# Kernel optimization log

Hardware: AMD Instinct MI355X
Metric: run time of the kernel (lower is better)

Reference implementation:

```python
import jax, jax.numpy as jnp
import numpy as np
from jax import lax

NSTEPS = 7
BN_EPS = 1e-5


def setup_inputs() -> dict:
    key = jax.random.key(0)
    ks = jax.random.split(key, 7)
    bs, in_ch, h, w, k = 8, 16, 256, 256, 3
    f = jax.random.normal(ks[0], (bs, in_ch, h, w), dtype=jnp.float32)
    vec_w = jax.random.normal(ks[1], (2 * in_ch, in_ch, k, k), dtype=jnp.float32) * 0.1
    vec_b = jax.random.normal(ks[2], (2 * in_ch,), dtype=jnp.float32) * 0.1
    bn_gamma = jnp.ones((2 * in_ch,), dtype=jnp.float32)
    bn_beta = jnp.zeros((2 * in_ch,), dtype=jnp.float32)
    fuse_w = jax.random.normal(ks[3], (in_ch, in_ch, NSTEPS, 1, 1), dtype=jnp.float32) * 0.1
    fuse_b = jax.random.normal(ks[4], (in_ch,), dtype=jnp.float32) * 0.1
    return {"f": f, "vec_w": vec_w, "vec_b": vec_b, "bn_gamma": bn_gamma,
            "bn_beta": bn_beta, "fuse_w": fuse_w, "fuse_b": fuse_b}


def _bilinear_sample(src, py, px):
    """Bilinear sample with zero padding (torch grid_sample align_corners=True).
    src: [N,C,H,W]; py,px: [N,H,W] pixel coordinates (row, col)."""
    N, C, H, W = src.shape
    y0 = jnp.floor(py); x0 = jnp.floor(px)
    wy1 = py - y0; wy0 = 1.0 - wy1
    wx1 = px - x0; wx0 = 1.0 - wx1
    src_flat = src.reshape(N, C, H * W)

    def gather(yi, xi):
        valid = (yi >= 0) & (yi <= H - 1) & (xi >= 0) & (xi <= W - 1)
        yc = jnp.clip(yi, 0, H - 1).astype(jnp.int32)
        xc = jnp.clip(xi, 0, W - 1).astype(jnp.int32)
        idx = (yc * W + xc).reshape(N, 1, H * W)
        vals = jnp.take_along_axis(src_flat, idx, axis=2).reshape(N, C, H, W)
        return vals * valid.astype(src.dtype)[:, None, :, :]

    out = (wy0 * wx0)[:, None] * gather(y0, x0) \
        + (wy0 * wx1)[:, None] * gather(y0, x0 + 1) \
        + (wy1 * wx0)[:, None] * gather(y0 + 1, x0) \
        + (wy1 * wx1)[:, None] * gather(y0 + 1, x0 + 1)
    return out


def _warp(src, flow, grid_y, grid_x):
    # grid + flow in pixel space; original normalizes to [-1,1] then grid_sample
    # un-normalizes with align_corners=True, which is exactly pixel coords grid+flow.
    py = grid_y[None] + flow[:, 0]
    px = grid_x[None] + flow[:, 1]
    return _bilinear_sample(src, py, px)


def reference(f, vec_w, vec_b, bn_gamma, bn_beta, fuse_w, fuse_b):
    bs, in_ch, h, w = f.shape
    # vec_conv + BatchNorm2d (training-mode batch stats, biased variance)
    vec = lax.conv_general_dilated(f, vec_w, (1, 1), [(1, 1), (1, 1)],
                                   dimension_numbers=("NCHW", "OIHW", "NCHW"))
    vec = vec + vec_b[None, :, None, None]
    mean = vec.mean(axis=(0, 2, 3))
    var = vec.var(axis=(0, 2, 3))
    vec = bn_gamma[None, :, None, None] * (vec - mean[None, :, None, None]) \
        * lax.rsqrt(var + BN_EPS)[None, :, None, None] + bn_beta[None, :, None, None]

    c = vec.shape[1]  # = 2*in_ch
    vec = vec.reshape(bs * c // 2, 2, h, w)  # per-channel 2D flow fields

    grid_y, grid_x = jnp.meshgrid(jnp.arange(h, dtype=f.dtype),
                                  jnp.arange(w, dtype=f.dtype), indexing="ij")

    # VecInt: scaling and squaring, keeping every intermediate deformation
    vec = vec * (1.0 / 2 ** NSTEPS)
    deforms = []
    for _ in range(NSTEPS):
        vec = vec + _warp(vec, vec, grid_y, grid_x)
        deforms.append(vec)

    fsrc = f.reshape(bs * in_ch, 1, h, w)
    maps = [_warp(fsrc, d, grid_y, grid_x).reshape(bs, in_ch, h, w) for d in deforms]
    stacked = jnp.stack(maps, axis=2)  # [bs, in_ch, nsteps, h, w]

    # Conv3d with kernel (nsteps,1,1) then squeeze -> per-pixel channel/step mix
    out = jnp.einsum("ocs,bcshw->bohw", fuse_w[:, :, :, 0, 0], stacked)
    out = out + fuse_b[None, :, None, None]
    return out
```

## Files before the change

kernel.cpp:

```cpp
#include <hip/hip_runtime.h>
#include <hip/hip_fp16.h>

#define H 256
#define W 256
#define BS 8
#define IC 16
#define OCH 32
#define NSTEPS 7
#define PLANE (H*W)
#define NFIELDS (BS*IC)
#define BN_N (BS*PLANE)
#define BN_EPS 1e-5f

__global__ void transpose_w_kernel(const float* __restrict__ w,
                                   float* __restrict__ wT) {
    for (int idx = threadIdx.x; idx < OCH * IC * 9; idx += blockDim.x) {
        int oc  = idx / (IC * 9);
        int rem = idx - oc * (IC * 9);
        wT[rem * OCH + oc] = w[idx];
    }
}

__global__ __launch_bounds__(256, 4) void conv_kernel(
    const float* __restrict__ f, const float* __restrict__ wT,
    const float* __restrict__ vec_b, __half2* __restrict__ vec_out,
    __half* __restrict__ f16c) {
    __shared__ float sf[8][18][34];

    int blk = blockIdx.x;
    int xcd = blk & 7;
    int i   = blk >> 3;
    int b   = i >> 4;
    int j   = i & 15;
    int ty0 = ((xcd << 1) | (j >> 3)) * 16;
    int tx0 = (j & 7) * 32;
    int tid = threadIdx.x;
    int tyl = tid >> 5, txl = tid & 31;
    int y0p = ty0 + tyl, y1p = ty0 + tyl + 8, x = tx0 + txl;

    float acc0[OCH], acc1[OCH];
#pragma unroll
    for (int oc = 0; oc < OCH; ++oc) { acc0[oc] = vec_b[oc]; acc1[oc] = vec_b[oc]; }

    for (int half = 0; half < 2; ++half) {
        if (half) __syncthreads();
        for (int idx = tid; idx < 8 * 18 * 34; idx += 256) {
            int ic = idx / 612;
            int r2 = idx - ic * 612;
            int r  = r2 / 34;
            int cc = r2 - r * 34;
            int gy = ty0 - 1 + r, gx = tx0 - 1 + cc;
            float v = 0.f;
            if (gy >= 0 && gy < H && gx >= 0 && gx < W)
                v = f[((size_t)(b * IC + half * 8 + ic) * H + gy) * W + gx];
            sf[ic][r][cc] = v;
        }
        __syncthreads();

#pragma unroll 2
        for (int ic = 0; ic < 8; ++ic) {
            size_t fb16 = (size_t)(b * IC + half * 8 + ic) * PLANE;
            f16c[fb16 + y0p * W + x] = __float2half(sf[ic][tyl + 1][txl + 1]);
            f16c[fb16 + y1p * W + x] = __float2half(sf[ic][tyl + 9][txl + 1]);
#pragma unroll
            for (int k = 0; k < 9; ++k) {
                int ky = k / 3, kx = k - ky * 3;
                float fv0 = sf[ic][tyl + ky][txl + kx];
                float fv1 = sf[ic][tyl + 8 + ky][txl + kx];
                const float* wrow = wT + ((half * 8 + ic) * 9 + k) * OCH;
#pragma unroll
                for (int oc = 0; oc < OCH; ++oc) {
                    float wv = wrow[oc];
                    acc0[oc] = fmaf(fv0, wv, acc0[oc]);
                    acc1[oc] = fmaf(fv1, wv, acc1[oc]);
                }
            }
        }
    }

#pragma unroll
    for (int c = 0; c < IC; ++c) {
        size_t pb = (size_t)(b * IC + c) * PLANE;
        vec_out[pb + y0p * W + x] =
            __float22half2_rn(make_float2(acc0[2 * c], acc0[2 * c + 1]));
        vec_out[pb + y1p * W + x] =
            __float22half2_rn(make_float2(acc1[2 * c], acc1[2 * c + 1]));
    }
}

__global__ __launch_bounds__(256) void stats_kernel(
    const __half2* __restrict__ vec, float* __restrict__ stats) {
    int blk   = blockIdx.x;
    int n     = blk >> 4;
    int chunk = blk & 15;
    const __half2* p = vec + (size_t)n * PLANE + chunk * 4096;
    int tid = threadIdx.x;

    float s0 = 0.f, s1 = 0.f, q0 = 0.f, q1 = 0.f;
#pragma unroll 4
    for (int i = tid; i < 4096; i += 256) {
        float2 v = __half22float2(p[i]);
        s0 += v.x; s1 += v.y;
        q0 = fmaf(v.x, v.x, q0);
        q1 = fmaf(v.y, v.y, q1);
    }
#pragma unroll
    for (int off = 32; off > 0; off >>= 1) {
        s0 += __shfl_down(s0, off, 64);
        s1 += __shfl_down(s1, off, 64);
        q0 += __shfl_down(q0, off, 64);
        q1 += __shfl_down(q1, off, 64);
    }
    __shared__ float red[4][4];
    int wave = tid >> 6, lane = tid & 63;
    if (lane == 0) {
        red[wave][0] = s0; red[wave][1] = s1;
        red[wave][2] = q0; red[wave][3] = q1;
    }
    __syncthreads();
    if (tid == 0) {
        float t0 = 0.f, t1 = 0.f, t2 = 0.f, t3 = 0.f;
#pragma unroll
        for (int wv = 0; wv < 4; ++wv) {
            t0 += red[wv][0]; t1 += red[wv][1];
            t2 += red[wv][2]; t3 += red[wv][3];
        }
        int ch0 = 2 * (n & 15);
        atomicAdd(stats + ch0,          t0);
        atomicAdd(stats + ch0 + 1,      t1);
        atomicAdd(stats + 32 + ch0,     t2);
        atomicAdd(stats + 32 + ch0 + 1, t3);
    }
}

__global__ void finalize_kernel(const float* __restrict__ stats,
                                const float* __restrict__ gamma,
                                const float* __restrict__ beta,
                                float* __restrict__ AB) {
    int ch = threadIdx.x;
    if (ch < 2 * IC) {
        const float invN = 1.f / (float)BN_N;
        float mean = stats[ch] * invN;
        float var  = stats[32 + ch] * invN - mean * mean;
        float rs   = rsqrtf(var + BN_EPS);
        float a    = gamma[ch] * rs;
        AB[ch]      = a * (1.f / 128.f);
        AB[32 + ch] = (beta[ch] - a * mean) * (1.f / 128.f);
    }
}

__device__ __forceinline__ void tap_setup(float py, float px,
                                          int* o, float* wt) {
    float ffy = floorf(py), ffx = floorf(px);
    int y0 = (int)ffy, x0 = (int)ffx;
    float wy1 = py - ffy, wy0 = 1.f - wy1;
    float wx1 = px - ffx, wx0 = 1.f - wx1;
    bool vy0 = (unsigned)y0 < (unsigned)H, vy1 = (unsigned)(y0 + 1) < (unsigned)H;
    bool vx0 = (unsigned)x0 < (unsigned)W, vx1 = (unsigned)(x0 + 1) < (unsigned)W;
    int yc0 = min(max(y0, 0), H - 1), yc1 = min(max(y0 + 1, 0), H - 1);
    int xc0 = min(max(x0, 0), W - 1), xc1 = min(max(x0 + 1, 0), W - 1);
    o[0] = yc0 * W + xc0; o[1] = yc0 * W + xc1;
    o[2] = yc1 * W + xc0; o[3] = yc1 * W + xc1;
    wt[0] = (vy0 && vx0) ? wy0 * wx0 : 0.f;
    wt[1] = (vy0 && vx1) ? wy0 * wx1 : 0.f;
    wt[2] = (vy1 && vx0) ? wy1 * wx0 : 0.f;
    wt[3] = (vy1 && vx1) ? wy1 * wx1 : 0.f;
}

template <bool FIRST, bool LAST>
__global__ __launch_bounds__(256) void step_kernel(
    const __half2* __restrict__ vin, __half2* __restrict__ vout,
    const __half* __restrict__ f16c, const float* __restrict__ AB,
    const float* __restrict__ fw, const float* __restrict__ fb,
    __half* __restrict__ accp, float* __restrict__ out, int step) {
    int blk = blockIdx.x;
    int xcd = blk & 7;
    int i   = blk >> 3;
    int b   = i >> 5;
    int h   = (xcd << 5) | (i & 31);
    int tx  = threadIdx.x;
    int idx = h * W + tx;
    const size_t base = (size_t)b * IC * PLANE;

    float mv[IC];

#pragma unroll 2
    for (int g = 0; g < 4; ++g) {
        float a0j[4], b0j[4], a1j[4], b1j[4];
        float fy[4], fx[4];
        int   o[4][4];
        float wt[4][4];
        const __half2* pl[4];
        float2 vc[4];

#pragma unroll
        for (int j = 0; j < 4; ++j) {
            int c = 4 * g + j;
            pl[j] = vin + base + (size_t)c * PLANE;
            vc[j] = __half22float2(pl[j][idx]);
        }

#pragma unroll
        for (int j = 0; j < 4; ++j) {
            int c = 4 * g + j;
            if (FIRST) {
                a0j[j] = AB[2 * c];     b0j[j] = AB[32 + 2 * c];
                a1j[j] = AB[2 * c + 1]; b1j[j] = AB[32 + 2 * c + 1];
            }
            fy[j] = FIRST ? fmaf(a0j[j], vc[j].x, b0j[j]) : vc[j].x;
            fx[j] = FIRST ? fmaf(a1j[j], vc[j].y, b1j[j]) : vc[j].y;
            tap_setup((float)h + fy[j], (float)tx + fx[j], o[j], wt[j]);
        }

        float2 t[4][4];
#pragma unroll
        for (int j = 0; j < 4; ++j)
#pragma unroll
            for (int k = 0; k < 4; ++k)
                t[j][k] = __half22float2(pl[j][o[j][k]]);

        float ny[4], nx[4];
        int   po[4][4];
        float pw[4][4];
#pragma unroll
        for (int j = 0; j < 4; ++j) {
            int c = 4 * g + j;
            float Sy = wt[j][0] * t[j][0].x + wt[j][1] * t[j][1].x
                     + wt[j][2] * t[j][2].x + wt[j][3] * t[j][3].x;
            float Sx = wt[j][0] * t[j][0].y + wt[j][1] * t[j][1].y
                     + wt[j][2] * t[j][2].y + wt[j][3] * t[j][3].y;
            if (FIRST) {
                float Ws = wt[j][0] + wt[j][1] + wt[j][2] + wt[j][3];
                ny[j] = fy[j] + fmaf(a0j[j], Sy, b0j[j] * Ws);
                nx[j] = fx[j] + fmaf(a1j[j], Sx, b1j[j] * Ws);
            } else {
                ny[j] = fy[j] + Sy;
                nx[j] = fx[j] + Sx;
            }
            if (!LAST)
                vout[base + (size_t)c * PLANE + idx] =
                    __float22half2_rn(make_float2(ny[j], nx[j]));
            tap_setup((float)h + ny[j], (float)tx + nx[j], po[j], pw[j]);
        }

#pragma unroll
        for (int j = 0; j < 4; ++j) {
            int c = 4 * g + j;
            const __half* fp = f16c + base + (size_t)c * PLANE;
            mv[c] = pw[j][0] * __half2float(fp[po[j][0]])
                  + pw[j][1] * __half2float(fp[po[j][1]])
                  + pw[j][2] * __half2float(fp[po[j][2]])
                  + pw[j][3] * __half2float(fp[po[j][3]]);
        }
    }

    __half* ap = accp + ((size_t)b * PLANE + idx) * IC;
    float prev[IC];
    if (!FIRST) {
        float4 p0 = ((const float4*)ap)[0];
        float4 p1 = ((const float4*)ap)[1];
        const __half2* ph = (const __half2*)&p0;
#pragma unroll
        for (int k = 0; k < 4; ++k) {
            float2 v = __half22float2(ph[k]);
            prev[2 * k] = v.x; prev[2 * k + 1] = v.y;
        }
        const __half2* qh = (const __half2*)&p1;
#pragma unroll
        for (int k = 0; k < 4; ++k) {
            float2 v = __half22float2(qh[k]);
            prev[8 + 2 * k] = v.x; prev[8 + 2 * k + 1] = v.y;
        }
    }

    float a[IC];
#pragma unroll
    for (int o2 = 0; o2 < IC; ++o2) {
        a[o2] = FIRST ? fb[o2] : prev[o2];
#pragma unroll
        for (int c = 0; c < IC; ++c)
            a[o2] = fmaf(fw[(o2 * IC + c) * NSTEPS + step], mv[c], a[o2]);
    }

    if (LAST) {
#pragma unroll
        for (int o2 = 0; o2 < IC; ++o2)
            out[base + (size_t)o2 * PLANE + idx] = a[o2];
    } else {
        float4 s0, s1;
        __half2* sh = (__half2*)&s0;
#pragma unroll
        for (int k = 0; k < 4; ++k)
            sh[k] = __float22half2_rn(make_float2(a[2 * k], a[2 * k + 1]));
        __half2* th = (__half2*)&s1;
#pragma unroll
        for (int k = 0; k < 4; ++k)
            th[k] = __float22half2_rn(make_float2(a[8 + 2 * k], a[9 + 2 * k]));
        ((float4*)ap)[0] = s0;
        ((float4*)ap)[1] = s1;
    }
}

extern "C" void kernel_launch(void* const* d_in, const int* in_sizes, int n_in,
                              void* d_out, int out_size, void* d_ws,
                              size_t ws_size, hipStream_t stream) {
    const float* f      = (const float*)d_in[0];
    const float* vec_w  = (const float*)d_in[1];
    const float* vec_b  = (const float*)d_in[2];
    const float* gamma  = (const float*)d_in[3];
    const float* beta   = (const float*)d_in[4];
    const float* fuse_w = (const float*)d_in[5];
    const float* fuse_b = (const float*)d_in[6];
    float* out = (float*)d_out;

    char* ws = (char*)d_ws;
    const size_t fieldBytes2 = (size_t)NFIELDS * PLANE * sizeof(__half2);
    const size_t fieldBytes1 = (size_t)NFIELDS * PLANE * sizeof(__half);
    __half2* buf0 = (__half2*)ws;
    __half2* buf1 = (__half2*)(ws + fieldBytes2);
    __half*  f16c = (__half*)(ws + 2 * fieldBytes2);
    __half*  accp = (__half*)(ws + 2 * fieldBytes2 + fieldBytes1);
    float*   wT   = (float*)(ws + 2 * fieldBytes2 + 2 * fieldBytes1);
    float*   stats = wT + OCH * IC * 9;
    float*   AB    = stats + 64;

    hipMemsetAsync(stats, 0, 64 * sizeof(float), stream);
    transpose_w_kernel<<<1, 512, 0, stream>>>(vec_w, wT);
    conv_kernel<<<1024, 256, 0, stream>>>(f, wT, vec_b, buf0, f16c);
    stats_kernel<<<NFIELDS * 16, 256, 0, stream>>>(buf0, stats);
    finalize_kernel<<<1, 64, 0, stream>>>(stats, gamma, beta, AB);

    __half2* vin = buf0;
    __half2* vout = buf1;
    for (int s = 0; s < NSTEPS; ++s) {
        if (s == 0)
            step_kernel<true, false><<<2048, 256, 0, stream>>>(
                vin, vout, f16c, AB, fuse_w, fuse_b, accp, out, s);
        else if (s < NSTEPS - 1)
            step_kernel<false, false><<<2048, 256, 0, stream>>>(
                vin, vout, f16c, AB, fuse_w, fuse_b, accp, out, s);
        else
            step_kernel<false, true><<<2048, 256, 0, stream>>>(
                vin, vout, f16c, AB, fuse_w, fuse_b, accp, out, s);
        __half2* t = vin; vin = vout; vout = t;
    }
}
```

Before: 560.7 us.

## Pad warp fields with zero guard border and use fp16 packed conv math

Step-kernel flow fields and the fp16 copy of f are stored in 260x260 planes with a zeroed one-pixel border. Bilinear taps then clamp coordinates into [-1,256] and read four neighbours at a single base offset, with no per-tap validity checks or index clamps. A new kernel zeroes the guard borders each launch. The 3x3 conv also switches from fp32 FMAs to packed half2 FMAs with half2 weights and fp16 shared memory, which loses accumulation precision ahead of BatchNorm.

```diff
diff --git a/kernel.cpp b/kernel.cpp
--- a/kernel.cpp
+++ b/kernel.cpp
@@ -11,21 +11,49 @@
 #define NFIELDS (BS*IC)
 #define BN_N (BS*PLANE)
 #define BN_EPS 1e-5f
+#define PW 260
+#define PSZ (260 * 260)
 
 __global__ void transpose_w_kernel(const float* __restrict__ w,
-                                   float* __restrict__ wT) {
-    for (int idx = threadIdx.x; idx < OCH * IC * 9; idx += blockDim.x) {
-        int oc  = idx / (IC * 9);
-        int rem = idx - oc * (IC * 9);
-        wT[rem * OCH + oc] = w[idx];
+                                   __half2* __restrict__ wTh) {
+    for (int idx = threadIdx.x; idx < IC * 9 * 16; idx += blockDim.x) {
+        int rc = idx >> 4;
+        int p  = idx & 15;
+        float lo = w[(2 * p) * (IC * 9) + rc];
+        float hi = w[(2 * p + 1) * (IC * 9) + rc];
+        wTh[idx] = __floats2half2_rn(lo, hi);
+    }
+}
+
+__global__ void guard_zero_kernel(unsigned* __restrict__ bufA,
+                                  unsigned* __restrict__ bufB,
+                                  unsigned short* __restrict__ f16p) {
+    int p = blockIdx.x;
+    size_t pb = (size_t)p * PSZ;
+    for (int i = threadIdx.x; i < 2064; i += blockDim.x) {
+        int row, col;
+        if (i < 1040) {
+            int r = i / 260;
+            row = (r == 0) ? 0 : 256 + r;
+            col = i - r * 260;
+        } else {
+            int j = i - 1040;
+            int c = j / 256;
+            col = (c == 0) ? 0 : 256 + c;
+            row = 1 + (j - c * 256);
+        }
+        size_t off = pb + (size_t)row * PW + col;
+        bufA[off] = 0u;
+        bufB[off] = 0u;
+        f16p[off] = 0;
     }
 }
 
 __global__ __launch_bounds__(256, 4) void conv_kernel(
-    const float* __restrict__ f, const float* __restrict__ wT,
+    const float* __restrict__ f, const __half2* __restrict__ wTh,
     const float* __restrict__ vec_b, __half2* __restrict__ vec_out,
-    __half* __restrict__ f16c) {
-    __shared__ float sf[8][18][34];
+    __half* __restrict__ f16p) {
+    __shared__ __half sf[8][18][34];
 
     int blk = blockIdx.x;
     int xcd = blk & 7;
@@ -38,9 +66,12 @@
     int tyl = tid >> 5, txl = tid & 31;
     int y0p = ty0 + tyl, y1p = ty0 + tyl + 8, x = tx0 + txl;
 
-    float acc0[OCH], acc1[OCH];
-#pragma unroll
-    for (int oc = 0; oc < OCH; ++oc) { acc0[oc] = vec_b[oc]; acc1[oc] = vec_b[oc]; }
+    __half2 acc0[16], acc1[16];
+#pragma unroll
+    for (int p = 0; p < 16; ++p) {
+        __half2 bp = __floats2half2_rn(vec_b[2 * p], vec_b[2 * p + 1]);
+        acc0[p] = bp; acc1[p] = bp;
+    }
 
     for (int half = 0; half < 2; ++half) {
         if (half) __syncthreads();
@@ -53,26 +84,26 @@
             float v = 0.f;
             if (gy >= 0 && gy < H && gx >= 0 && gx < W)
                 v = f[((size_t)(b * IC + half * 8 + ic) * H + gy) * W + gx];
-            sf[ic][r][cc] = v;
+            sf[ic][r][cc] = __float2half(v);
         }
         __syncthreads();
 
 #pragma unroll 2
         for (int ic = 0; ic < 8; ++ic) {
-            size_t fb16 = (size_t)(b * IC + half * 8 + ic) * PLANE;
-            f16c[fb16 + y0p * W + x] = __float2half(sf[ic][tyl + 1][txl + 1]);
-            f16c[fb16 + y1p * W + x] = __float2half(sf[ic][tyl + 9][txl + 1]);
+            size_t fb16 = (size_t)(b * IC + half * 8 + ic) * PSZ;
+            f16p[fb16 + (size_t)(y0p + 1) * PW + x + 1] = sf[ic][tyl + 1][txl + 1];
+            f16p[fb16 + (size_t)(y1p + 1) * PW + x + 1] = sf[ic][tyl + 9][txl + 1];
 #pragma unroll
             for (int k = 0; k < 9; ++k) {
                 int ky = k / 3, kx = k - ky * 3;
-                float fv0 = sf[ic][tyl + ky][txl + kx];
-                float fv1 = sf[ic][tyl + 8 + ky][txl + kx];
-                const float* wrow = wT + ((half * 8 + ic) * 9 + k) * OCH;
-#pragma unroll
-                for (int oc = 0; oc < OCH; ++oc) {
-                    float wv = wrow[oc];
-                    acc0[oc] = fmaf(fv0, wv, acc0[oc]);
-                    acc1[oc] = fmaf(fv1, wv, acc1[oc]);
+                __half2 fv0 = __half2half2(sf[ic][tyl + ky][txl + kx]);
+                __half2 fv1 = __half2half2(sf[ic][tyl + 8 + ky][txl + kx]);
+                const __half2* wrow = wTh + ((half * 8 + ic) * 9 + k) * 16;
+#pragma unroll
+                for (int p = 0; p < 16; ++p) {
+                    __half2 wv = wrow[p];
+                    acc0[p] = __hfma2(fv0, wv, acc0[p]);
+                    acc1[p] = __hfma2(fv1, wv, acc1[p]);
                 }
             }
         }
@@ -81,10 +112,8 @@
 #pragma unroll
     for (int c = 0; c < IC; ++c) {
         size_t pb = (size_t)(b * IC + c) * PLANE;
-        vec_out[pb + y0p * W + x] =
-            __float22half2_rn(make_float2(acc0[2 * c], acc0[2 * c + 1]));
-        vec_out[pb + y1p * W + x] =
-            __float22half2_rn(make_float2(acc1[2 * c], acc1[2 * c + 1]));
+        vec_out[pb + y0p * W + x] = acc0[c];
+        vec_out[pb + y1p * W + x] = acc1[c];
     }
 }
 
@@ -167,20 +196,36 @@
     wt[3] = (vy1 && vx1) ? wy1 * wx1 : 0.f;
 }
 
+__device__ __forceinline__ void tap_fast(float py, float px,
+                                         int& o, float* wt) {
+    float pyc = fminf(fmaxf(py, -1.f), 256.f);
+    float pxc = fminf(fmaxf(px, -1.f), 256.f);
+    float fy = floorf(pyc), fx = floorf(pxc);
+    int y0 = (int)fy, x0 = (int)fx;
+    float wy1 = pyc - fy, wy0 = 1.f - wy1;
+    float wx1 = pxc - fx, wx0 = 1.f - wx1;
+    o = (y0 + 1) * PW + (x0 + 1);
+    wt[0] = wy0 * wx0; wt[1] = wy0 * wx1;
+    wt[2] = wy1 * wx0; wt[3] = wy1 * wx1;
+}
+
 template <bool FIRST, bool LAST>
 __global__ __launch_bounds__(256) void step_kernel(
-    const __half2* __restrict__ vin, __half2* __restrict__ vout,
-    const __half* __restrict__ f16c, const float* __restrict__ AB,
-    const float* __restrict__ fw, const float* __restrict__ fb,
-    __half* __restrict__ accp, float* __restrict__ out, int step) {
+    const __half2* __restrict__ vinRaw, const __half2* __restrict__ vinPad,
+    __half2* __restrict__ voutPad, const __half* __restrict__ f16p,
+    const float* __restrict__ AB, const float* __restrict__ fw,
+    const float* __restrict__ fb, __half* __restrict__ accp,
+    float* __restrict__ out, int step) {
     int blk = blockIdx.x;
     int xcd = blk & 7;
     int i   = blk >> 3;
     int b   = i >> 5;
     int h   = (xcd << 5) | (i & 31);
     int tx  = threadIdx.x;
-    int idx = h * W + tx;
-    const size_t base = (size_t)b * IC * PLANE;
+    int idx_raw = h * W + tx;
+    int idx_pad = (h + 1) * PW + tx + 1;
+    const size_t baseR = (size_t)b * IC * PLANE;
+    const size_t baseP = (size_t)b * IC * PSZ;
 
     float mv[IC];
 
@@ -188,16 +233,22 @@
     for (int g = 0; g < 4; ++g) {
         float a0j[4], b0j[4], a1j[4], b1j[4];
         float fy[4], fx[4];
-        int   o[4][4];
         float wt[4][4];
+        int   ob[4];
+        int   om[4][4];
         const __half2* pl[4];
         float2 vc[4];
 
 #pragma unroll
         for (int j = 0; j < 4; ++j) {
             int c = 4 * g + j;
-            pl[j] = vin + base + (size_t)c * PLANE;
-            vc[j] = __half22float2(pl[j][idx]);
+            if (FIRST) {
+                pl[j] = vinRaw + baseR + (size_t)c * PLANE;
+                vc[j] = __half22float2(pl[j][idx_raw]);
+            } else {
+                pl[j] = vinPad + baseP + (size_t)c * PSZ;
+                vc[j] = __half22float2(pl[j][idx_pad]);
+            }
         }
 
 #pragma unroll
@@ -206,22 +257,34 @@
             if (FIRST) {
                 a0j[j] = AB[2 * c];     b0j[j] = AB[32 + 2 * c];
                 a1j[j] = AB[2 * c + 1]; b1j[j] = AB[32 + 2 * c + 1];
+                fy[j] = fmaf(a0j[j], vc[j].x, b0j[j]);
+                fx[j] = fmaf(a1j[j], vc[j].y, b1j[j]);
+                tap_setup((float)h + fy[j], (float)tx + fx[j], om[j], wt[j]);
+            } else {
+                fy[j] = vc[j].x;
+                fx[j] = vc[j].y;
+                tap_fast((float)h + fy[j], (float)tx + fx[j], ob[j], wt[j]);
             }
-            fy[j] = FIRST ? fmaf(a0j[j], vc[j].x, b0j[j]) : vc[j].x;
-            fx[j] = FIRST ? fmaf(a1j[j], vc[j].y, b1j[j]) : vc[j].y;
-            tap_setup((float)h + fy[j], (float)tx + fx[j], o[j], wt[j]);
         }
 
         float2 t[4][4];
 #pragma unroll
-        for (int j = 0; j < 4; ++j)
-#pragma unroll
-            for (int k = 0; k < 4; ++k)
-                t[j][k] = __half22float2(pl[j][o[j][k]]);
+        for (int j = 0; j < 4; ++j) {
+            if (FIRST) {
+#pragma unroll
+                for (int k = 0; k < 4; ++k)
+                    t[j][k] = __half22float2(pl[j][om[j][k]]);
+            } else {
+                t[j][0] = __half22float2(pl[j][ob[j]]);
+                t[j][1] = __half22float2(pl[j][ob[j] + 1]);
+                t[j][2] = __half22float2(pl[j][ob[j] + PW]);
+                t[j][3] = __half22float2(pl[j][ob[j] + PW + 1]);
+            }
+        }
 
         float ny[4], nx[4];
-        int   po[4][4];
-        float pw[4][4];
+        int   pb_[4];
+        float pw_[4][4];
 #pragma unroll
         for (int j = 0; j < 4; ++j) {
             int c = 4 * g + j;
@@ -238,23 +301,23 @@
                 nx[j] = fx[j] + Sx;
             }
             if (!LAST)
-                vout[base + (size_t)c * PLANE + idx] =
+                voutPad[baseP + (size_t)c * PSZ + idx_pad] =
                     __float22half2_rn(make_float2(ny[j], nx[j]));
-            tap_setup((float)h + ny[j], (float)tx + nx[j], po[j], pw[j]);
+            tap_fast((float)h + ny[j], (float)tx + nx[j], pb_[j], pw_[j]);
         }
 
 #pragma unroll
         for (int j = 0; j < 4; ++j) {
             int c = 4 * g + j;
-            const __half* fp = f16c + base + (size_t)c * PLANE;
-            mv[c] = pw[j][0] * __half2float(fp[po[j][0]])
-                  + pw[j][1] * __half2float(fp[po[j][1]])
-                  + pw[j][2] * __half2float(fp[po[j][2]])
-                  + pw[j][3] * __half2float(fp[po[j][3]]);
-        }
-    }
-
-    __half* ap = accp + ((size_t)b * PLANE + idx) * IC;
+            const __half* fp = f16p + baseP + (size_t)c * PSZ;
+            mv[c] = pw_[j][0] * __half2float(fp[pb_[j]])
+                  + pw_[j][1] * __half2float(fp[pb_[j] + 1])
+                  + pw_[j][2] * __half2float(fp[pb_[j] + PW])
+                  + pw_[j][3] * __half2float(fp[pb_[j] + PW + 1]);
+        }
+    }
+
+    __half* ap = accp + ((size_t)b * PLANE + idx_raw) * IC;
     float prev[IC];
     if (!FIRST) {
         float4 p0 = ((const float4*)ap)[0];
@@ -285,7 +348,7 @@
     if (LAST) {
 #pragma unroll
         for (int o2 = 0; o2 < IC; ++o2)
-            out[base + (size_t)o2 * PLANE + idx] = a[o2];
+            out[baseR + (size_t)o2 * PLANE + idx_raw] = a[o2];
     } else {
         float4 s0, s1;
         __half2* sh = (__half2*)&s0;
@@ -314,34 +377,41 @@
     float* out = (float*)d_out;
 
     char* ws = (char*)d_ws;
-    const size_t fieldBytes2 = (size_t)NFIELDS * PLANE * sizeof(__half2);
-    const size_t fieldBytes1 = (size_t)NFIELDS * PLANE * sizeof(__half);
-    __half2* buf0 = (__half2*)ws;
-    __half2* buf1 = (__half2*)(ws + fieldBytes2);
-    __half*  f16c = (__half*)(ws + 2 * fieldBytes2);
-    __half*  accp = (__half*)(ws + 2 * fieldBytes2 + fieldBytes1);
-    float*   wT   = (float*)(ws + 2 * fieldBytes2 + 2 * fieldBytes1);
-    float*   stats = wT + OCH * IC * 9;
-    float*   AB    = stats + 64;
+    const size_t rawB  = (size_t)NFIELDS * PLANE * sizeof(__half2);
+    const size_t padB2 = (size_t)NFIELDS * PSZ * sizeof(__half2);
+    const size_t padB1 = (size_t)NFIELDS * PSZ * sizeof(__half);
+    const size_t accB  = (size_t)NFIELDS * PLANE * sizeof(__half);
+    __half2* bufRaw = (__half2*)ws;
+    __half2* bufA   = (__half2*)(ws + rawB);
+    __half2* bufB   = (__half2*)(ws + rawB + padB2);
+    __half*  f16p   = (__half*)(ws + rawB + 2 * padB2);
+    __half*  accp   = (__half*)(ws + rawB + 2 * padB2 + padB1);
+    __half2* wTh    = (__half2*)(ws + rawB + 2 * padB2 + padB1 + accB);
+    float*   stats  = (float*)(wTh + IC * 9 * 16);
+    float*   AB     = stats + 64;
 
     hipMemsetAsync(stats, 0, 64 * sizeof(float), stream);
-    transpose_w_kernel<<<1, 512, 0, stream>>>(vec_w, wT);
-    conv_kernel<<<1024, 256, 0, stream>>>(f, wT, vec_b, buf0, f16c);
-    stats_kernel<<<NFIELDS * 16, 256, 0, stream>>>(buf0, stats);
+    transpose_w_kernel<<<1, 512, 0, stream>>>(vec_w, wTh);
+    guard_zero_kernel<<<NFIELDS, 256, 0, stream>>>(
+        (unsigned*)bufA, (unsigned*)bufB, (unsigned short*)f16p);
+    conv_kernel<<<1024, 256, 0, stream>>>(f, wTh, vec_b, bufRaw, f16p);
+    stats_kernel<<<NFIELDS * 16, 256, 0, stream>>>(bufRaw, stats);
     finalize_kernel<<<1, 64, 0, stream>>>(stats, gamma, beta, AB);
 
-    __half2* vin = buf0;
-    __half2* vout = buf1;
     for (int s = 0; s < NSTEPS; ++s) {
+        const __half2* vinPad = (s & 1) ? bufA : bufB;
+        __half2*       voutP  = (s & 1) ? bufB : bufA;
         if (s == 0)
             step_kernel<true, false><<<2048, 256, 0, stream>>>(
-                vin, vout, f16c, AB, fuse_w, fuse_b, accp, out, s);
+                bufRaw, (const __half2*)nullptr, bufA, f16p, AB,
+                fuse_w, fuse_b, accp, out, s);
         else if (s < NSTEPS - 1)
             step_kernel<false, false><<<2048, 256, 0, stream>>>(
-                vin, vout, f16c, AB, fuse_w, fuse_b, accp, out, s);
+                (const __half2*)nullptr, vinPad, voutP, f16p, AB,
+                fuse_w, fuse_b, accp, out, s);
         else
             step_kernel<false, true><<<2048, 256, 0, stream>>>(
-                vin, vout, f16c, AB, fuse_w, fuse_b, accp, out, s);
-        __half2* t = vin; vin = vout; vout = t;
-    }
-}
+                (const __half2*)nullptr, vinPad, (__half2*)nullptr, f16p, AB,
+                fuse_w, fuse_b, accp, out, s);
+    }
+}
```

Measured after the change: 500.7 us. 10.7% less time.
